# Performance work log

Measured on AMD Instinct MI355X. Metric: run time of the kernel, lower is better.

## Reference

```python
import jax, jax.numpy as jnp
import numpy as np

N = 50000      # nodes
E = 800000     # edges (avg degree 16)
D_IN = 128
D_OUT = 128


def setup_inputs() -> dict:
    key = jax.random.key(0)
    k = jax.random.split(key, 6)
    x = jax.random.normal(k[0], (N, D_IN), dtype=jnp.float32)
    rows = jax.random.randint(k[1], (E,), 0, N, dtype=jnp.int32)   # destination nodes
    cols = jax.random.randint(k[2], (E,), 0, N, dtype=jnp.int32)   # source nodes
    vals = jax.random.uniform(k[3], (E,), dtype=jnp.float32)       # adj edge weights
    W = jax.random.normal(k[4], (D_OUT, D_IN), dtype=jnp.float32) * (1.0 / np.sqrt(D_IN))
    b = jax.random.normal(k[5], (D_OUT,), dtype=jnp.float32) * 0.01
    return {"x": x, "rows": rows, "cols": cols, "vals": vals, "W": W, "b": b}


def reference(x, rows, cols, vals, W, b):
    # Linear: h = x @ W^T + b   (torch nn.Linear convention, W: [out, in])
    h = jnp.einsum("ni,oi->no", x, W) + b            # [N, D_OUT]
    # spmm(adj, h): out[i] = sum_{(i,j) in E} vals_ij * h[j]
    msgs = h[cols] * vals[:, None]                    # [E, D_OUT]
    out = jax.ops.segment_sum(msgs, rows, num_segments=N)  # [N, D_OUT]
    return out
```

## Files before the change

### kernel.cpp

```cpp
#include <hip/hip_runtime.h>

#define D 128
#define SCAN_BLK 256
#define SCAN_THREADS 1024

typedef short  bf16x8 __attribute__((ext_vector_type(8)));
typedef float  f32x4  __attribute__((ext_vector_type(4)));

static __device__ __forceinline__ unsigned short f2bf(float f) {
    unsigned u = __float_as_uint(f);
    u += 0x7FFFu + ((u >> 16) & 1u);
    return (unsigned short)(u >> 16);
}
static __device__ __forceinline__ float bf2f_lo(unsigned u) {
    return __uint_as_float((u & 0xFFFFu) << 16);
}
static __device__ __forceinline__ float bf2f_hi(unsigned u) {
    return __uint_as_float(u & 0xFFFF0000u);
}

__global__ __launch_bounds__(256) void fused_pre(
    const int* __restrict__ rows, int* __restrict__ counts, int n_edges,
    const float* __restrict__ W, unsigned short* __restrict__ Wb, int histBlocks) {
    int bid = blockIdx.x;
    if (bid < histBlocks) {
        int i = bid * 256 + threadIdx.x;
        if (i < n_edges) atomicAdd(&counts[rows[i]], 1);
    } else {
        int i = (bid - histBlocks) * 256 + threadIdx.x;
        if (i < D * D) Wb[i] = f2bf(W[i]);
    }
}

__global__ __launch_bounds__(256) void fused_main(
    const int* __restrict__ rows, const int* __restrict__ cols,
    const float* __restrict__ vals, int* __restrict__ cursor,
    int2* __restrict__ evec, int n_edges, int permSlots,
    const float* __restrict__ x, const unsigned short* __restrict__ Wb,
    const float* __restrict__ b, unsigned short* __restrict__ hb, int n_rows) {
    const int bid = blockIdx.x;
    const int g   = bid / 5;
    const int r5  = bid % 5;

    if (r5 >= 2) {
        const int slot   = g * 3 + (r5 - 2);
        const int stride = permSlots * 256;
        for (int i = slot * 256 + threadIdx.x; i < n_edges; i += stride) {
            int rr  = rows[i];
            int pos = atomicAdd(&cursor[rr], 1);
            evec[pos] = make_int2(cols[i], __float_as_int(vals[i]));
        }
        return;
    }

    const int gb   = g * 2 + r5;
    const int lane = threadIdx.x & 63;
    const int wv   = threadIdx.x >> 6;
    const int row0 = gb * 64 + wv * 16;
    if (row0 >= n_rows) return;
    const int m  = lane & 15;
    const int kg = lane >> 4;

    int arow = row0 + m;
    if (arow >= n_rows) arow = n_rows - 1;
    const float* xr = x + (size_t)arow * D + kg * 8;

    f32x4 acc[8];
#pragma unroll
    for (int n = 0; n < 8; ++n) acc[n] = (f32x4){0.f, 0.f, 0.f, 0.f};

#pragma unroll
    for (int ks = 0; ks < 4; ++ks) {
        float4 f0 = *(const float4*)(xr + ks * 32);
        float4 f1 = *(const float4*)(xr + ks * 32 + 4);
        bf16x8 a;
        a[0] = (short)f2bf(f0.x); a[1] = (short)f2bf(f0.y);
        a[2] = (short)f2bf(f0.z); a[3] = (short)f2bf(f0.w);
        a[4] = (short)f2bf(f1.x); a[5] = (short)f2bf(f1.y);
        a[6] = (short)f2bf(f1.z); a[7] = (short)f2bf(f1.w);
#pragma unroll
        for (int n = 0; n < 8; ++n) {
            bf16x8 bf = *(const bf16x8*)&Wb[(size_t)(n * 16 + m) * D + ks * 32 + kg * 8];
            acc[n] = __builtin_amdgcn_mfma_f32_16x16x32_bf16(a, bf, acc[n], 0, 0, 0);
        }
    }

#pragma unroll
    for (int n = 0; n < 8; ++n) {
        int col = n * 16 + m;
        float bc = b[col];
#pragma unroll
        for (int j = 0; j < 4; ++j) {
            int rr = row0 + kg * 4 + j;
            if (rr < n_rows) hb[(size_t)rr * D + col] = f2bf(acc[n][j] + bc);
        }
    }
}

__global__ __launch_bounds__(SCAN_BLK) void scan_local(
    const int* __restrict__ counts, int* __restrict__ offs,
    int* __restrict__ blockSums, int n) {
    __shared__ int sh[SCAN_BLK];
    const int t = threadIdx.x;
    const int i = blockIdx.x * SCAN_BLK + t;
    int v = (i < n) ? counts[i] : 0;
    sh[t] = v;
    __syncthreads();
    for (int off = 1; off < SCAN_BLK; off <<= 1) {
        int add = (t >= off) ? sh[t - off] : 0;
        __syncthreads();
        sh[t] += add;
        __syncthreads();
    }
    if (i < n) offs[i] = sh[t] - v;
    if (t == SCAN_BLK - 1) blockSums[blockIdx.x] = sh[SCAN_BLK - 1];
}

__global__ __launch_bounds__(1024) void scan_blocks(
    int* __restrict__ blockSums, int* __restrict__ total, int nb) {
    __shared__ int sh[1024];
    const int t = threadIdx.x;
    int v = (t < nb) ? blockSums[t] : 0;
    sh[t] = v;
    __syncthreads();
    for (int off = 1; off < 1024; off <<= 1) {
        int add = (t >= off) ? sh[t - off] : 0;
        __syncthreads();
        sh[t] += add;
        __syncthreads();
    }
    if (t < nb) blockSums[t] = sh[t] - v;
    if (t == 1023) *total = sh[1023];
}

__global__ __launch_bounds__(SCAN_BLK) void scan_add(
    int* __restrict__ offs, int* __restrict__ cursor,
    const int* __restrict__ blockSums, int n) {
    const int i = blockIdx.x * SCAN_BLK + threadIdx.x;
    if (i < n) {
        int o = offs[i] + blockSums[blockIdx.x];
        offs[i]   = o;
        cursor[i] = o;
    }
}

__global__ __launch_bounds__(SCAN_THREADS) void scan_counts(
    const int* __restrict__ counts, int* __restrict__ offs,
    int* __restrict__ cursor, int n) {
    __shared__ int part[SCAN_THREADS];
    const int t = threadIdx.x;
    const int chunk = (n + SCAN_THREADS - 1) / SCAN_THREADS;
    const int s = t * chunk;
    const int e = min(s + chunk, n);
    int sum = 0;
    for (int i = s; i < e; ++i) sum += counts[i];
    part[t] = sum;
    __syncthreads();
    for (int off = 1; off < SCAN_THREADS; off <<= 1) {
        int add = (t >= off) ? part[t - off] : 0;
        __syncthreads();
        part[t] += add;
        __syncthreads();
    }
    int run = part[t] - sum;
    for (int i = s; i < e; ++i) {
        offs[i]   = run;
        cursor[i] = run;
        run += counts[i];
    }
    if (e == n) offs[n] = run;
}

__global__ __launch_bounds__(256, 4) void aggregate(
    const int* __restrict__ offs, const int2* __restrict__ evec,
    const unsigned short* __restrict__ hb, float* __restrict__ out, int n_nodes) {
    const int lane = threadIdx.x & 63;
    const int hl   = lane >> 5;
    const int node = (blockIdx.x * 4 + (threadIdx.x >> 6)) * 2 + hl;
    const int c0   = (lane & 31) * 4;

    int s = 0, e = 0;
    if (node < n_nodes) { s = offs[node]; e = offs[node + 1]; }
    const int rounds = (e - s + 7) >> 3;

    float4 acc = make_float4(0.f, 0.f, 0.f, 0.f);

    for (int rd = 0; rd < rounds; ++rd) {
        const int k = s + rd * 8;
        const int em1 = e - 1;
        int2 r0 = evec[min(k + 0, em1)];
        int2 r1 = evec[min(k + 1, em1)];
        int2 r2 = evec[min(k + 2, em1)];
        int2 r3 = evec[min(k + 3, em1)];
        int2 r4 = evec[min(k + 4, em1)];
        int2 r5 = evec[min(k + 5, em1)];
        int2 r6 = evec[min(k + 6, em1)];
        int2 r7 = evec[min(k + 7, em1)];
        uint2 u0 = *(const uint2*)&hb[(size_t)r0.x * D + c0];
        uint2 u1 = *(const uint2*)&hb[(size_t)r1.x * D + c0];
        uint2 u2 = *(const uint2*)&hb[(size_t)r2.x * D + c0];
        uint2 u3 = *(const uint2*)&hb[(size_t)r3.x * D + c0];
        uint2 u4 = *(const uint2*)&hb[(size_t)r4.x * D + c0];
        uint2 u5 = *(const uint2*)&hb[(size_t)r5.x * D + c0];
        uint2 u6 = *(const uint2*)&hb[(size_t)r6.x * D + c0];
        uint2 u7 = *(const uint2*)&hb[(size_t)r7.x * D + c0];
        float v0 = (k + 0 < e) ? __int_as_float(r0.y) : 0.f;
        float v1 = (k + 1 < e) ? __int_as_float(r1.y) : 0.f;
        float v2 = (k + 2 < e) ? __int_as_float(r2.y) : 0.f;
        float v3 = (k + 3 < e) ? __int_as_float(r3.y) : 0.f;
        float v4 = (k + 4 < e) ? __int_as_float(r4.y) : 0.f;
        float v5 = (k + 5 < e) ? __int_as_float(r5.y) : 0.f;
        float v6 = (k + 6 < e) ? __int_as_float(r6.y) : 0.f;
        float v7 = (k + 7 < e) ? __int_as_float(r7.y) : 0.f;
        acc.x += v0 * bf2f_lo(u0.x); acc.y += v0 * bf2f_hi(u0.x);
        acc.z += v0 * bf2f_lo(u0.y); acc.w += v0 * bf2f_hi(u0.y);
        acc.x += v1 * bf2f_lo(u1.x); acc.y += v1 * bf2f_hi(u1.x);
        acc.z += v1 * bf2f_lo(u1.y); acc.w += v1 * bf2f_hi(u1.y);
        acc.x += v2 * bf2f_lo(u2.x); acc.y += v2 * bf2f_hi(u2.x);
        acc.z += v2 * bf2f_lo(u2.y); acc.w += v2 * bf2f_hi(u2.y);
        acc.x += v3 * bf2f_lo(u3.x); acc.y += v3 * bf2f_hi(u3.x);
        acc.z += v3 * bf2f_lo(u3.y); acc.w += v3 * bf2f_hi(u3.y);
        acc.x += v4 * bf2f_lo(u4.x); acc.y += v4 * bf2f_hi(u4.x);
        acc.z += v4 * bf2f_lo(u4.y); acc.w += v4 * bf2f_hi(u4.y);
        acc.x += v5 * bf2f_lo(u5.x); acc.y += v5 * bf2f_hi(u5.x);
        acc.z += v5 * bf2f_lo(u5.y); acc.w += v5 * bf2f_hi(u5.y);
        acc.x += v6 * bf2f_lo(u6.x); acc.y += v6 * bf2f_hi(u6.x);
        acc.z += v6 * bf2f_lo(u6.y); acc.w += v6 * bf2f_hi(u6.y);
        acc.x += v7 * bf2f_lo(u7.x); acc.y += v7 * bf2f_hi(u7.x);
        acc.z += v7 * bf2f_lo(u7.y); acc.w += v7 * bf2f_hi(u7.y);
    }

    if (node < n_nodes)
        *(float4*)&out[(size_t)node * D + c0] = acc;
}

__global__ __launch_bounds__(256) void scatter_add(
    const int* __restrict__ rows, const int* __restrict__ cols,
    const float* __restrict__ vals, const unsigned short* __restrict__ hb,
    float* __restrict__ out, int n_edges) {
    long long gid = (long long)blockIdx.x * blockDim.x + threadIdx.x;
    int e  = (int)(gid >> 5);
    if (e >= n_edges) return;
    int d4 = ((int)gid & 31) * 4;
    int   r = rows[e];
    int   c = cols[e];
    float v = vals[e];
    const unsigned short* hp = &hb[(size_t)c * D + d4];
    unsigned u0 = *(const unsigned*)(hp + 0);
    unsigned u1 = *(const unsigned*)(hp + 2);
    float* op = &out[(size_t)r * D + d4];
    atomicAdd(op + 0, v * bf2f_lo(u0));
    atomicAdd(op + 1, v * bf2f_hi(u0));
    atomicAdd(op + 2, v * bf2f_lo(u1));
    atomicAdd(op + 3, v * bf2f_hi(u1));
}

__global__ void convert_W(const float* __restrict__ W, unsigned short* __restrict__ Wb) {
    int i = blockIdx.x * blockDim.x + threadIdx.x;
    if (i < D * D) Wb[i] = f2bf(W[i]);
}

__global__ __launch_bounds__(256) void gemm_mfma(
    const float* __restrict__ x, const unsigned short* __restrict__ Wb,
    const float* __restrict__ b, unsigned short* __restrict__ hb, int n_rows) {
    const int lane = threadIdx.x & 63;
    const int wv   = threadIdx.x >> 6;
    const int row0 = blockIdx.x * 64 + wv * 16;
    if (row0 >= n_rows) return;
    const int m  = lane & 15;
    const int kg = lane >> 4;
    int arow = row0 + m;
    if (arow >= n_rows) arow = n_rows - 1;
    const float* xr = x + (size_t)arow * D + kg * 8;
    f32x4 acc[8];
#pragma unroll
    for (int n = 0; n < 8; ++n) acc[n] = (f32x4){0.f, 0.f, 0.f, 0.f};
#pragma unroll
    for (int ks = 0; ks < 4; ++ks) {
        float4 f0 = *(const float4*)(xr + ks * 32);
        float4 f1 = *(const float4*)(xr + ks * 32 + 4);
        bf16x8 a;
        a[0] = (short)f2bf(f0.x); a[1] = (short)f2bf(f0.y);
        a[2] = (short)f2bf(f0.z); a[3] = (short)f2bf(f0.w);
        a[4] = (short)f2bf(f1.x); a[5] = (short)f2bf(f1.y);
        a[6] = (short)f2bf(f1.z); a[7] = (short)f2bf(f1.w);
#pragma unroll
        for (int n = 0; n < 8; ++n) {
            bf16x8 bf = *(const bf16x8*)&Wb[(size_t)(n * 16 + m) * D + ks * 32 + kg * 8];
            acc[n] = __builtin_amdgcn_mfma_f32_16x16x32_bf16(a, bf, acc[n], 0, 0, 0);
        }
    }
#pragma unroll
    for (int n = 0; n < 8; ++n) {
        int col = n * 16 + m;
        float bc = b[col];
#pragma unroll
        for (int j = 0; j < 4; ++j) {
            int r = row0 + kg * 4 + j;
            if (r < n_rows) hb[(size_t)r * D + col] = f2bf(acc[n][j] + bc);
        }
    }
}

static inline size_t align16(size_t x) { return (x + 15) & ~(size_t)15; }

extern "C" void kernel_launch(void* const* d_in, const int* in_sizes, int n_in,
                              void* d_out, int out_size, void* d_ws, size_t ws_size,
                              hipStream_t stream) {
    const float* x    = (const float*)d_in[0];
    const int*   rows = (const int*)  d_in[1];
    const int*   cols = (const int*)  d_in[2];
    const float* vals = (const float*)d_in[3];
    const float* W    = (const float*)d_in[4];
    const float* b    = (const float*)d_in[5];
    float*       out  = (float*)d_out;

    const int n_nodes = in_sizes[0] / D;
    const int n_edges = in_sizes[1];
    const int nScanBlocks = (n_nodes + SCAN_BLK - 1) / SCAN_BLK;
    const int histBlocks  = (n_edges + 255) / 256;
    const int convBlocks  = (D * D + 255) / 256;
    const int gemmBlocks  = (n_nodes + 63) / 64;
    const int nGroups     = (gemmBlocks + 1) / 2;
    const int permSlots   = nGroups * 3;
    const int mainBlocks  = nGroups * 5;
    const int aggBlocks   = (n_nodes + 7) / 8;

    char*  base    = (char*)d_ws;
    size_t off     = 0;
    unsigned short* Wb = (unsigned short*)(base + off); off = align16(off + (size_t)D * D * 2);
    unsigned short* hb = (unsigned short*)(base + off); off = align16(off + (size_t)n_nodes * D * 2);
    int*   counts  = (int*)  (base + off); off = align16(off + (size_t)n_nodes * 4);
    int*   offs    = (int*)  (base + off); off = align16(off + ((size_t)n_nodes + 1) * 4);
    int*   cursor  = (int*)  (base + off); off = align16(off + (size_t)n_nodes * 4);
    int*   bsums   = (int*)  (base + off); off = align16(off + (size_t)1024 * 4);
    int2*  evec    = (int2*) (base + off); off = align16(off + (size_t)n_edges * 8);
    const bool csr_fits = (off <= ws_size);

    if (csr_fits) {
        hipMemsetAsync(counts, 0, (size_t)n_nodes * 4, stream);
        fused_pre<<<histBlocks + convBlocks, 256, 0, stream>>>(
            rows, counts, n_edges, W, Wb, histBlocks);
        if (nScanBlocks <= 1024) {
            scan_local<<<nScanBlocks, SCAN_BLK, 0, stream>>>(counts, offs, bsums, n_nodes);
            scan_blocks<<<1, 1024, 0, stream>>>(bsums, &offs[n_nodes], nScanBlocks);
            scan_add<<<nScanBlocks, SCAN_BLK, 0, stream>>>(offs, cursor, bsums, n_nodes);
        } else {
            scan_counts<<<1, SCAN_THREADS, 0, stream>>>(counts, offs, cursor, n_nodes);
        }
        fused_main<<<mainBlocks, 256, 0, stream>>>(
            rows, cols, vals, cursor, evec, n_edges, permSlots,
            x, Wb, b, hb, n_nodes);
        aggregate<<<aggBlocks, 256, 0, stream>>>(offs, evec, hb, out, n_nodes);
    } else {
        convert_W<<<convBlocks, 256, 0, stream>>>(W, Wb);
        gemm_mfma<<<gemmBlocks, 256, 0, stream>>>(x, Wb, b, hb, n_nodes);
        hipMemsetAsync(d_out, 0, (size_t)n_nodes * D * sizeof(float), stream);
        long long scatter_threads = (long long)n_edges * 32;
        int scatter_blocks = (int)((scatter_threads + 255) / 256);
        scatter_add<<<scatter_blocks, 256, 0, stream>>>(rows, cols, vals, hb, out, n_edges);
    }
}
```

Before: 144.1 us.

## Partition CSR build into eight XCD-aligned edge classes with per-class cursors

Edges are split into eight classes by 256-edge chunk index. Histogram and permutation blocks are arranged so that block index mod 8 matches the class, and each class uses its own count and cursor arrays (class-major, eight times n_nodes). The intent is that each class's atomics and evec writes stay within one XCD's L2, avoiding cross-die atomic traffic. The cost is an eight-times-larger scan, and an aggregate that reads eight per-class segments per node and runs for the largest class count. Those extra rounds issue padded, redundant gathers.

```diff
diff --git a/kernel.cpp b/kernel.cpp
--- a/kernel.cpp
+++ b/kernel.cpp
@@ -2,7 +2,6 @@
 
 #define D 128
 #define SCAN_BLK 256
-#define SCAN_THREADS 1024
 
 typedef short  bf16x8 __attribute__((ext_vector_type(8)));
 typedef float  f32x4  __attribute__((ext_vector_type(4)));
@@ -20,80 +19,19 @@
 }
 
 __global__ __launch_bounds__(256) void fused_pre(
-    const int* __restrict__ rows, int* __restrict__ counts, int n_edges,
+    const int* __restrict__ rows, int* __restrict__ counts8,
+    int n_edges, int n_nodes,
     const float* __restrict__ W, unsigned short* __restrict__ Wb, int histBlocks) {
     int bid = blockIdx.x;
     if (bid < histBlocks) {
         int i = bid * 256 + threadIdx.x;
-        if (i < n_edges) atomicAdd(&counts[rows[i]], 1);
+        if (i < n_edges) {
+            int cls = (i >> 8) & 7;
+            atomicAdd(&counts8[cls * n_nodes + rows[i]], 1);
+        }
     } else {
         int i = (bid - histBlocks) * 256 + threadIdx.x;
         if (i < D * D) Wb[i] = f2bf(W[i]);
-    }
-}
-
-__global__ __launch_bounds__(256) void fused_main(
-    const int* __restrict__ rows, const int* __restrict__ cols,
-    const float* __restrict__ vals, int* __restrict__ cursor,
-    int2* __restrict__ evec, int n_edges, int permSlots,
-    const float* __restrict__ x, const unsigned short* __restrict__ Wb,
-    const float* __restrict__ b, unsigned short* __restrict__ hb, int n_rows) {
-    const int bid = blockIdx.x;
-    const int g   = bid / 5;
-    const int r5  = bid % 5;
-
-    if (r5 >= 2) {
-        const int slot   = g * 3 + (r5 - 2);
-        const int stride = permSlots * 256;
-        for (int i = slot * 256 + threadIdx.x; i < n_edges; i += stride) {
-            int rr  = rows[i];
-            int pos = atomicAdd(&cursor[rr], 1);
-            evec[pos] = make_int2(cols[i], __float_as_int(vals[i]));
-        }
-        return;
-    }
-
-    const int gb   = g * 2 + r5;
-    const int lane = threadIdx.x & 63;
-    const int wv   = threadIdx.x >> 6;
-    const int row0 = gb * 64 + wv * 16;
-    if (row0 >= n_rows) return;
-    const int m  = lane & 15;
-    const int kg = lane >> 4;
-
-    int arow = row0 + m;
-    if (arow >= n_rows) arow = n_rows - 1;
-    const float* xr = x + (size_t)arow * D + kg * 8;
-
-    f32x4 acc[8];
-#pragma unroll
-    for (int n = 0; n < 8; ++n) acc[n] = (f32x4){0.f, 0.f, 0.f, 0.f};
-
-#pragma unroll
-    for (int ks = 0; ks < 4; ++ks) {
-        float4 f0 = *(const float4*)(xr + ks * 32);
-        float4 f1 = *(const float4*)(xr + ks * 32 + 4);
-        bf16x8 a;
-        a[0] = (short)f2bf(f0.x); a[1] = (short)f2bf(f0.y);
-        a[2] = (short)f2bf(f0.z); a[3] = (short)f2bf(f0.w);
-        a[4] = (short)f2bf(f1.x); a[5] = (short)f2bf(f1.y);
-        a[6] = (short)f2bf(f1.z); a[7] = (short)f2bf(f1.w);
-#pragma unroll
-        for (int n = 0; n < 8; ++n) {
-            bf16x8 bf = *(const bf16x8*)&Wb[(size_t)(n * 16 + m) * D + ks * 32 + kg * 8];
-            acc[n] = __builtin_amdgcn_mfma_f32_16x16x32_bf16(a, bf, acc[n], 0, 0, 0);
-        }
-    }
-
-#pragma unroll
-    for (int n = 0; n < 8; ++n) {
-        int col = n * 16 + m;
-        float bc = b[col];
-#pragma unroll
-        for (int j = 0; j < 4; ++j) {
-            int rr = row0 + kg * 4 + j;
-            if (rr < n_rows) hb[(size_t)rr * D + col] = f2bf(acc[n][j] + bc);
-        }
     }
 }
 
@@ -116,12 +54,13 @@
     if (t == SCAN_BLK - 1) blockSums[blockIdx.x] = sh[SCAN_BLK - 1];
 }
 
-__global__ __launch_bounds__(1024) void scan_blocks(
+__global__ __launch_bounds__(1024) void scan_blocks2(
     int* __restrict__ blockSums, int* __restrict__ total, int nb) {
     __shared__ int sh[1024];
     const int t = threadIdx.x;
-    int v = (t < nb) ? blockSums[t] : 0;
-    sh[t] = v;
+    int c0 = (t * 2     < nb) ? blockSums[t * 2]     : 0;
+    int c1 = (t * 2 + 1 < nb) ? blockSums[t * 2 + 1] : 0;
+    sh[t] = c0 + c1;
     __syncthreads();
     for (int off = 1; off < 1024; off <<= 1) {
         int add = (t >= off) ? sh[t - off] : 0;
@@ -129,7 +68,9 @@
         sh[t] += add;
         __syncthreads();
     }
-    if (t < nb) blockSums[t] = sh[t] - v;
+    int base = sh[t] - (c0 + c1);
+    if (t * 2 < nb)     blockSums[t * 2]     = base;
+    if (t * 2 + 1 < nb) blockSums[t * 2 + 1] = base + c0;
     if (t == 1023) *total = sh[1023];
 }
 
@@ -144,94 +85,177 @@
     }
 }
 
-__global__ __launch_bounds__(SCAN_THREADS) void scan_counts(
-    const int* __restrict__ counts, int* __restrict__ offs,
-    int* __restrict__ cursor, int n) {
-    __shared__ int part[SCAN_THREADS];
-    const int t = threadIdx.x;
-    const int chunk = (n + SCAN_THREADS - 1) / SCAN_THREADS;
-    const int s = t * chunk;
-    const int e = min(s + chunk, n);
-    int sum = 0;
-    for (int i = s; i < e; ++i) sum += counts[i];
-    part[t] = sum;
-    __syncthreads();
-    for (int off = 1; off < SCAN_THREADS; off <<= 1) {
-        int add = (t >= off) ? part[t - off] : 0;
-        __syncthreads();
-        part[t] += add;
-        __syncthreads();
-    }
-    int run = part[t] - sum;
-    for (int i = s; i < e; ++i) {
-        offs[i]   = run;
-        cursor[i] = run;
-        run += counts[i];
-    }
-    if (e == n) offs[n] = run;
+__global__ __launch_bounds__(256) void fused_main(
+    const int* __restrict__ rows, const int* __restrict__ cols,
+    const float* __restrict__ vals, int* __restrict__ cursor8,
+    int2* __restrict__ evec, int n_edges, int n_nodes,
+    int nChunks, int QperClass,
+    const float* __restrict__ x, const unsigned short* __restrict__ Wb,
+    const float* __restrict__ b, unsigned short* __restrict__ hb, int n_rows) {
+    const int bid = blockIdx.x;
+    const int r5  = bid % 5;
+
+    if (r5 >= 2) {
+        const int k   = bid & 7;
+        const int S   = bid / 40;
+        const int pos = bid % 40;
+        int r = 0;
+        for (int p = 0; p < pos; ++p)
+            if ((p % 5) >= 2 && (p & 7) == k) ++r;
+        const int q = S * 3 + r;
+        for (int m = q; ; m += QperClass) {
+            int c = k + 8 * m;
+            if (c >= nChunks) break;
+            int i = c * 256 + threadIdx.x;
+            if (i < n_edges) {
+                int rr  = rows[i];
+                int pp  = atomicAdd(&cursor8[k * n_nodes + rr], 1);
+                evec[pp] = make_int2(cols[i], __float_as_int(vals[i]));
+            }
+        }
+        return;
+    }
+
+    const int gb   = (bid / 5) * 2 + r5;
+    const int lane = threadIdx.x & 63;
+    const int wv   = threadIdx.x >> 6;
+    const int row0 = gb * 64 + wv * 16;
+    if (row0 >= n_rows) return;
+    const int m  = lane & 15;
+    const int kg = lane >> 4;
+
+    int arow = row0 + m;
+    if (arow >= n_rows) arow = n_rows - 1;
+    const float* xr = x + (size_t)arow * D + kg * 8;
+
+    f32x4 acc[8];
+#pragma unroll
+    for (int n = 0; n < 8; ++n) acc[n] = (f32x4){0.f, 0.f, 0.f, 0.f};
+
+#pragma unroll
+    for (int ks = 0; ks < 4; ++ks) {
+        float4 f0 = *(const float4*)(xr + ks * 32);
+        float4 f1 = *(const float4*)(xr + ks * 32 + 4);
+        bf16x8 a;
+        a[0] = (short)f2bf(f0.x); a[1] = (short)f2bf(f0.y);
+        a[2] = (short)f2bf(f0.z); a[3] = (short)f2bf(f0.w);
+        a[4] = (short)f2bf(f1.x); a[5] = (short)f2bf(f1.y);
+        a[6] = (short)f2bf(f1.z); a[7] = (short)f2bf(f1.w);
+#pragma unroll
+        for (int n = 0; n < 8; ++n) {
+            bf16x8 bf = *(const bf16x8*)&Wb[(size_t)(n * 16 + m) * D + ks * 32 + kg * 8];
+            acc[n] = __builtin_amdgcn_mfma_f32_16x16x32_bf16(a, bf, acc[n], 0, 0, 0);
+        }
+    }
+
+#pragma unroll
+    for (int n = 0; n < 8; ++n) {
+        int col = n * 16 + m;
+        float bc = b[col];
+#pragma unroll
+        for (int j = 0; j < 4; ++j) {
+            int rr = row0 + kg * 4 + j;
+            if (rr < n_rows) hb[(size_t)rr * D + col] = f2bf(acc[n][j] + bc);
+        }
+    }
 }
 
 __global__ __launch_bounds__(256, 4) void aggregate(
-    const int* __restrict__ offs, const int2* __restrict__ evec,
-    const unsigned short* __restrict__ hb, float* __restrict__ out, int n_nodes) {
+    const int* __restrict__ offs8, const int2* __restrict__ evec,
+    const unsigned short* __restrict__ hb, float* __restrict__ out,
+    int n_nodes, int n_edges) {
     const int lane = threadIdx.x & 63;
     const int hl   = lane >> 5;
     const int node = (blockIdx.x * 4 + (threadIdx.x >> 6)) * 2 + hl;
     const int c0   = (lane & 31) * 4;
 
-    int s = 0, e = 0;
-    if (node < n_nodes) { s = offs[node]; e = offs[node + 1]; }
-    const int rounds = (e - s + 7) >> 3;
+    int s[8], cnt[8];
+    int rounds = 0;
+    if (node < n_nodes) {
+#pragma unroll
+        for (int c = 0; c < 8; ++c) {
+            int a  = offs8[c * n_nodes + node];
+            int bd = offs8[c * n_nodes + node + 1];
+            s[c]   = a;
+            cnt[c] = bd - a;
+            rounds = max(rounds, cnt[c]);
+        }
+    } else {
+#pragma unroll
+        for (int c = 0; c < 8; ++c) { s[c] = 0; cnt[c] = 0; }
+    }
 
     float4 acc = make_float4(0.f, 0.f, 0.f, 0.f);
+    const int emax = n_edges - 1;
 
     for (int rd = 0; rd < rounds; ++rd) {
-        const int k = s + rd * 8;
-        const int em1 = e - 1;
-        int2 r0 = evec[min(k + 0, em1)];
-        int2 r1 = evec[min(k + 1, em1)];
-        int2 r2 = evec[min(k + 2, em1)];
-        int2 r3 = evec[min(k + 3, em1)];
-        int2 r4 = evec[min(k + 4, em1)];
-        int2 r5 = evec[min(k + 5, em1)];
-        int2 r6 = evec[min(k + 6, em1)];
-        int2 r7 = evec[min(k + 7, em1)];
-        uint2 u0 = *(const uint2*)&hb[(size_t)r0.x * D + c0];
-        uint2 u1 = *(const uint2*)&hb[(size_t)r1.x * D + c0];
-        uint2 u2 = *(const uint2*)&hb[(size_t)r2.x * D + c0];
-        uint2 u3 = *(const uint2*)&hb[(size_t)r3.x * D + c0];
-        uint2 u4 = *(const uint2*)&hb[(size_t)r4.x * D + c0];
-        uint2 u5 = *(const uint2*)&hb[(size_t)r5.x * D + c0];
-        uint2 u6 = *(const uint2*)&hb[(size_t)r6.x * D + c0];
-        uint2 u7 = *(const uint2*)&hb[(size_t)r7.x * D + c0];
-        float v0 = (k + 0 < e) ? __int_as_float(r0.y) : 0.f;
-        float v1 = (k + 1 < e) ? __int_as_float(r1.y) : 0.f;
-        float v2 = (k + 2 < e) ? __int_as_float(r2.y) : 0.f;
-        float v3 = (k + 3 < e) ? __int_as_float(r3.y) : 0.f;
-        float v4 = (k + 4 < e) ? __int_as_float(r4.y) : 0.f;
-        float v5 = (k + 5 < e) ? __int_as_float(r5.y) : 0.f;
-        float v6 = (k + 6 < e) ? __int_as_float(r6.y) : 0.f;
-        float v7 = (k + 7 < e) ? __int_as_float(r7.y) : 0.f;
-        acc.x += v0 * bf2f_lo(u0.x); acc.y += v0 * bf2f_hi(u0.x);
-        acc.z += v0 * bf2f_lo(u0.y); acc.w += v0 * bf2f_hi(u0.y);
-        acc.x += v1 * bf2f_lo(u1.x); acc.y += v1 * bf2f_hi(u1.x);
-        acc.z += v1 * bf2f_lo(u1.y); acc.w += v1 * bf2f_hi(u1.y);
-        acc.x += v2 * bf2f_lo(u2.x); acc.y += v2 * bf2f_hi(u2.x);
-        acc.z += v2 * bf2f_lo(u2.y); acc.w += v2 * bf2f_hi(u2.y);
-        acc.x += v3 * bf2f_lo(u3.x); acc.y += v3 * bf2f_hi(u3.x);
-        acc.z += v3 * bf2f_lo(u3.y); acc.w += v3 * bf2f_hi(u3.y);
-        acc.x += v4 * bf2f_lo(u4.x); acc.y += v4 * bf2f_hi(u4.x);
-        acc.z += v4 * bf2f_lo(u4.y); acc.w += v4 * bf2f_hi(u4.y);
-        acc.x += v5 * bf2f_lo(u5.x); acc.y += v5 * bf2f_hi(u5.x);
-        acc.z += v5 * bf2f_lo(u5.y); acc.w += v5 * bf2f_hi(u5.y);
-        acc.x += v6 * bf2f_lo(u6.x); acc.y += v6 * bf2f_hi(u6.x);
-        acc.z += v6 * bf2f_lo(u6.y); acc.w += v6 * bf2f_hi(u6.y);
-        acc.x += v7 * bf2f_lo(u7.x); acc.y += v7 * bf2f_hi(u7.x);
-        acc.z += v7 * bf2f_lo(u7.y); acc.w += v7 * bf2f_hi(u7.y);
+        int2  rec[8];
+#pragma unroll
+        for (int c = 0; c < 8; ++c) {
+            int idx = s[c] + min(rd, max(cnt[c] - 1, 0));
+            rec[c] = evec[min(idx, emax)];
+        }
+        uint2 u[8];
+#pragma unroll
+        for (int c = 0; c < 8; ++c)
+            u[c] = *(const uint2*)&hb[(size_t)rec[c].x * D + c0];
+#pragma unroll
+        for (int c = 0; c < 8; ++c) {
+            float v = (rd < cnt[c]) ? __int_as_float(rec[c].y) : 0.f;
+            acc.x += v * bf2f_lo(u[c].x); acc.y += v * bf2f_hi(u[c].x);
+            acc.z += v * bf2f_lo(u[c].y); acc.w += v * bf2f_hi(u[c].y);
+        }
     }
 
     if (node < n_nodes)
         *(float4*)&out[(size_t)node * D + c0] = acc;
+}
+
+__global__ void convert_W(const float* __restrict__ W, unsigned short* __restrict__ Wb) {
+    int i = blockIdx.x * blockDim.x + threadIdx.x;
+    if (i < D * D) Wb[i] = f2bf(W[i]);
+}
+
+__global__ __launch_bounds__(256) void gemm_mfma(
+    const float* __restrict__ x, const unsigned short* __restrict__ Wb,
+    const float* __restrict__ b, unsigned short* __restrict__ hb, int n_rows) {
+    const int lane = threadIdx.x & 63;
+    const int wv   = threadIdx.x >> 6;
+    const int row0 = blockIdx.x * 64 + wv * 16;
+    if (row0 >= n_rows) return;
+    const int m  = lane & 15;
+    const int kg = lane >> 4;
+    int arow = row0 + m;
+    if (arow >= n_rows) arow = n_rows - 1;
+    const float* xr = x + (size_t)arow * D + kg * 8;
+    f32x4 acc[8];
+#pragma unroll
+    for (int n = 0; n < 8; ++n) acc[n] = (f32x4){0.f, 0.f, 0.f, 0.f};
+#pragma unroll
+    for (int ks = 0; ks < 4; ++ks) {
+        float4 f0 = *(const float4*)(xr + ks * 32);
+        float4 f1 = *(const float4*)(xr + ks * 32 + 4);
+        bf16x8 a;
+        a[0] = (short)f2bf(f0.x); a[1] = (short)f2bf(f0.y);
+        a[2] = (short)f2bf(f0.z); a[3] = (short)f2bf(f0.w);
+        a[4] = (short)f2bf(f1.x); a[5] = (short)f2bf(f1.y);
+        a[6] = (short)f2bf(f1.z); a[7] = (short)f2bf(f1.w);
+#pragma unroll
+        for (int n = 0; n < 8; ++n) {
+            bf16x8 bf = *(const bf16x8*)&Wb[(size_t)(n * 16 + m) * D + ks * 32 + kg * 8];
+            acc[n] = __builtin_amdgcn_mfma_f32_16x16x32_bf16(a, bf, acc[n], 0, 0, 0);
+        }
+    }
+#pragma unroll
+    for (int n = 0; n < 8; ++n) {
+        int col = n * 16 + m;
+        float bc = b[col];
+#pragma unroll
+        for (int j = 0; j < 4; ++j) {
+            int r = row0 + kg * 4 + j;
+            if (r < n_rows) hb[(size_t)r * D + col] = f2bf(acc[n][j] + bc);
+        }
+    }
 }
 
 __global__ __launch_bounds__(256) void scatter_add(
@@ -255,53 +279,6 @@
     atomicAdd(op + 3, v * bf2f_hi(u1));
 }
 
-__global__ void convert_W(const float* __restrict__ W, unsigned short* __restrict__ Wb) {
-    int i = blockIdx.x * blockDim.x + threadIdx.x;
-    if (i < D * D) Wb[i] = f2bf(W[i]);
-}
-
-__global__ __launch_bounds__(256) void gemm_mfma(
-    const float* __restrict__ x, const unsigned short* __restrict__ Wb,
-    const float* __restrict__ b, unsigned short* __restrict__ hb, int n_rows) {
-    const int lane = threadIdx.x & 63;
-    const int wv   = threadIdx.x >> 6;
-    const int row0 = blockIdx.x * 64 + wv * 16;
-    if (row0 >= n_rows) return;
-    const int m  = lane & 15;
-    const int kg = lane >> 4;
-    int arow = row0 + m;
-    if (arow >= n_rows) arow = n_rows - 1;
-    const float* xr = x + (size_t)arow * D + kg * 8;
-    f32x4 acc[8];
-#pragma unroll
-    for (int n = 0; n < 8; ++n) acc[n] = (f32x4){0.f, 0.f, 0.f, 0.f};
-#pragma unroll
-    for (int ks = 0; ks < 4; ++ks) {
-        float4 f0 = *(const float4*)(xr + ks * 32);
-        float4 f1 = *(const float4*)(xr + ks * 32 + 4);
-        bf16x8 a;
-        a[0] = (short)f2bf(f0.x); a[1] = (short)f2bf(f0.y);
-        a[2] = (short)f2bf(f0.z); a[3] = (short)f2bf(f0.w);
-        a[4] = (short)f2bf(f1.x); a[5] = (short)f2bf(f1.y);
-        a[6] = (short)f2bf(f1.z); a[7] = (short)f2bf(f1.w);
-#pragma unroll
-        for (int n = 0; n < 8; ++n) {
-            bf16x8 bf = *(const bf16x8*)&Wb[(size_t)(n * 16 + m) * D + ks * 32 + kg * 8];
-            acc[n] = __builtin_amdgcn_mfma_f32_16x16x32_bf16(a, bf, acc[n], 0, 0, 0);
-        }
-    }
-#pragma unroll
-    for (int n = 0; n < 8; ++n) {
-        int col = n * 16 + m;
-        float bc = b[col];
-#pragma unroll
-        for (int j = 0; j < 4; ++j) {
-            int r = row0 + kg * 4 + j;
-            if (r < n_rows) hb[(size_t)r * D + col] = f2bf(acc[n][j] + bc);
-        }
-    }
-}
-
 static inline size_t align16(size_t x) { return (x + 15) & ~(size_t)15; }
 
 extern "C" void kernel_launch(void* const* d_in, const int* in_sizes, int n_in,
@@ -317,41 +294,39 @@
 
     const int n_nodes = in_sizes[0] / D;
     const int n_edges = in_sizes[1];
-    const int nScanBlocks = (n_nodes + SCAN_BLK - 1) / SCAN_BLK;
-    const int histBlocks  = (n_edges + 255) / 256;
-    const int convBlocks  = (D * D + 255) / 256;
-    const int gemmBlocks  = (n_nodes + 63) / 64;
-    const int nGroups     = (gemmBlocks + 1) / 2;
-    const int permSlots   = nGroups * 3;
-    const int mainBlocks  = nGroups * 5;
-    const int aggBlocks   = (n_nodes + 7) / 8;
+    const int histBlocks = (n_edges + 255) / 256;
+    const int convBlocks = (D * D + 255) / 256;
+    const int gemmBlocks = (n_nodes + 63) / 64;
+    const int nSuper     = (gemmBlocks + 15) / 16;
+    const int mainBlocks = nSuper * 40;
+    const int QperClass  = nSuper * 3;
+    const int n8         = 8 * n_nodes;
+    const int nScanBlocks = (n8 + SCAN_BLK - 1) / SCAN_BLK;
+    const int aggBlocks  = (n_nodes + 7) / 8;
 
     char*  base    = (char*)d_ws;
     size_t off     = 0;
     unsigned short* Wb = (unsigned short*)(base + off); off = align16(off + (size_t)D * D * 2);
     unsigned short* hb = (unsigned short*)(base + off); off = align16(off + (size_t)n_nodes * D * 2);
-    int*   counts  = (int*)  (base + off); off = align16(off + (size_t)n_nodes * 4);
-    int*   offs    = (int*)  (base + off); off = align16(off + ((size_t)n_nodes + 1) * 4);
-    int*   cursor  = (int*)  (base + off); off = align16(off + (size_t)n_nodes * 4);
-    int*   bsums   = (int*)  (base + off); off = align16(off + (size_t)1024 * 4);
+    int*   counts8 = (int*)  (base + off); off = align16(off + (size_t)n8 * 4);
+    int*   offs8   = (int*)  (base + off); off = align16(off + ((size_t)n8 + 1) * 4);
+    int*   cursor8 = (int*)  (base + off); off = align16(off + (size_t)n8 * 4);
+    int*   bsums   = (int*)  (base + off); off = align16(off + (size_t)2048 * 4);
     int2*  evec    = (int2*) (base + off); off = align16(off + (size_t)n_edges * 8);
-    const bool csr_fits = (off <= ws_size);
-
-    if (csr_fits) {
-        hipMemsetAsync(counts, 0, (size_t)n_nodes * 4, stream);
+    const bool ok = (off <= ws_size) && (nScanBlocks <= 2048);
+
+    if (ok) {
+        hipMemsetAsync(counts8, 0, (size_t)n8 * 4, stream);
         fused_pre<<<histBlocks + convBlocks, 256, 0, stream>>>(
-            rows, counts, n_edges, W, Wb, histBlocks);
-        if (nScanBlocks <= 1024) {
-            scan_local<<<nScanBlocks, SCAN_BLK, 0, stream>>>(counts, offs, bsums, n_nodes);
-            scan_blocks<<<1, 1024, 0, stream>>>(bsums, &offs[n_nodes], nScanBlocks);
-            scan_add<<<nScanBlocks, SCAN_BLK, 0, stream>>>(offs, cursor, bsums, n_nodes);
-        } else {
-            scan_counts<<<1, SCAN_THREADS, 0, stream>>>(counts, offs, cursor, n_nodes);
-        }
+            rows, counts8, n_edges, n_nodes, W, Wb, histBlocks);
+        scan_local<<<nScanBlocks, SCAN_BLK, 0, stream>>>(counts8, offs8, bsums, n8);
+        scan_blocks2<<<1, 1024, 0, stream>>>(bsums, &offs8[n8], nScanBlocks);
+        scan_add<<<nScanBlocks, SCAN_BLK, 0, stream>>>(offs8, cursor8, bsums, n8);
         fused_main<<<mainBlocks, 256, 0, stream>>>(
-            rows, cols, vals, cursor, evec, n_edges, permSlots,
-            x, Wb, b, hb, n_nodes);
-        aggregate<<<aggBlocks, 256, 0, stream>>>(offs, evec, hb, out, n_nodes);
+            rows, cols, vals, cursor8, evec, n_edges, n_nodes,
+            histBlocks, QperClass, x, Wb, b, hb, n_nodes);
+        aggregate<<<aggBlocks, 256, 0, stream>>>(
+            offs8, evec, hb, out, n_nodes, n_edges);
     } else {
         convert_W<<<convBlocks, 256, 0, stream>>>(W, Wb);
         gemm_mfma<<<gemmBlocks, 256, 0, stream>>>(x, Wb, b, hb, n_nodes);
```

After: 161.5 us. 12.1% more time.

## Fuse whole pipeline into one cooperative persistent kernel with grid syncs

Applied to the files above, without the earlier changes.

Replaces the sequence of memset, histogram, three scan kernels, permute+GEMM and aggregate launches with a single cooperative kernel that separates the phases with grid.sync(). GEMM tiles and the edge permutation run concurrently on disjoint block subsets. The aggregation is changed to one wave per node with two columns per lane instead of a half-wave with four. This is meant to remove launch gaps and inter-kernel drain, at the cost of grid-wide barriers, a grid size capped by occupancy, and narrower per-lane gathers. The atomic scatter fallback for a small workspace is removed, so the workspace-size check no longer exists.

```diff
diff --git a/kernel.cpp b/kernel.cpp
--- a/kernel.cpp
+++ b/kernel.cpp
@@ -1,8 +1,10 @@
 #include <hip/hip_runtime.h>
+#include <hip/hip_cooperative_groups.h>
+
+namespace cg = cooperative_groups;
 
 #define D 128
 #define SCAN_BLK 256
-#define SCAN_THREADS 1024
 
 typedef short  bf16x8 __attribute__((ext_vector_type(8)));
 typedef float  f32x4  __attribute__((ext_vector_type(4)));
@@ -17,6 +19,174 @@
 }
 static __device__ __forceinline__ float bf2f_hi(unsigned u) {
     return __uint_as_float(u & 0xFFFF0000u);
+}
+
+__global__ __launch_bounds__(256) void mega(
+    const int* __restrict__ rows, const int* __restrict__ cols,
+    const float* __restrict__ vals, const float* __restrict__ W,
+    const float* __restrict__ b, const float* __restrict__ x,
+    int* __restrict__ counts, int* __restrict__ offs, int* __restrict__ cursor,
+    int* __restrict__ bsums, int2* __restrict__ evec,
+    unsigned short* __restrict__ Wb, unsigned short* __restrict__ hb,
+    float* __restrict__ out,
+    int n_nodes, int n_edges, int nScanChunks, int gemmTiles, int gemmShare) {
+    cg::grid_group grid = cg::this_grid();
+    const int t   = threadIdx.x;
+    const int bid = blockIdx.x;
+    const int G   = gridDim.x;
+    const int gstride = G * 256;
+    __shared__ int sh[SCAN_BLK];
+
+    for (int i = bid * 256 + t; i < n_nodes; i += gstride) counts[i] = 0;
+    for (int i = bid * 256 + t; i < D * D;   i += gstride) Wb[i] = f2bf(W[i]);
+    grid.sync();
+
+    for (int i = bid * 256 + t; i < n_edges; i += gstride)
+        atomicAdd(&counts[rows[i]], 1);
+    grid.sync();
+
+    for (int ch = bid; ch < nScanChunks; ch += G) {
+        int i = ch * 256 + t;
+        int v = (i < n_nodes) ? counts[i] : 0;
+        sh[t] = v;
+        __syncthreads();
+        for (int off = 1; off < 256; off <<= 1) {
+            int add = (t >= off) ? sh[t - off] : 0;
+            __syncthreads();
+            sh[t] += add;
+            __syncthreads();
+        }
+        if (i < n_nodes) offs[i] = sh[t] - v;
+        if (t == 255) bsums[ch] = sh[255];
+        __syncthreads();
+    }
+    grid.sync();
+
+    if (bid == 0) {
+        int v = (t < nScanChunks) ? bsums[t] : 0;
+        sh[t] = v;
+        __syncthreads();
+        for (int off = 1; off < 256; off <<= 1) {
+            int add = (t >= off) ? sh[t - off] : 0;
+            __syncthreads();
+            sh[t] += add;
+            __syncthreads();
+        }
+        if (t < nScanChunks) bsums[t] = sh[t] - v;
+        if (t == 255) offs[n_nodes] = sh[255];
+    }
+    grid.sync();
+
+    for (int ch = bid; ch < nScanChunks; ch += G) {
+        int i = ch * 256 + t;
+        if (i < n_nodes) {
+            int o = offs[i] + bsums[ch];
+            offs[i]   = o;
+            cursor[i] = o;
+        }
+    }
+    grid.sync();
+
+    if (bid < gemmShare) {
+        const int lane = t & 63;
+        const int wv   = t >> 6;
+        const int m    = lane & 15;
+        const int kg   = lane >> 4;
+        for (int gb = bid; gb < gemmTiles; gb += gemmShare) {
+            const int row0 = gb * 64 + wv * 16;
+            if (row0 >= n_nodes) continue;
+            int arow = row0 + m;
+            if (arow >= n_nodes) arow = n_nodes - 1;
+            const float* xr = x + (size_t)arow * D + kg * 8;
+
+            f32x4 acc[8];
+#pragma unroll
+            for (int n = 0; n < 8; ++n) acc[n] = (f32x4){0.f, 0.f, 0.f, 0.f};
+#pragma unroll
+            for (int ks = 0; ks < 4; ++ks) {
+                float4 f0 = *(const float4*)(xr + ks * 32);
+                float4 f1 = *(const float4*)(xr + ks * 32 + 4);
+                bf16x8 a;
+                a[0] = (short)f2bf(f0.x); a[1] = (short)f2bf(f0.y);
+                a[2] = (short)f2bf(f0.z); a[3] = (short)f2bf(f0.w);
+                a[4] = (short)f2bf(f1.x); a[5] = (short)f2bf(f1.y);
+                a[6] = (short)f2bf(f1.z); a[7] = (short)f2bf(f1.w);
+#pragma unroll
+                for (int n = 0; n < 8; ++n) {
+                    bf16x8 bf = *(const bf16x8*)&Wb[(size_t)(n * 16 + m) * D + ks * 32 + kg * 8];
+                    acc[n] = __builtin_amdgcn_mfma_f32_16x16x32_bf16(a, bf, acc[n], 0, 0, 0);
+                }
+            }
+#pragma unroll
+            for (int n = 0; n < 8; ++n) {
+                int col = n * 16 + m;
+                float bc = b[col];
+#pragma unroll
+                for (int j = 0; j < 4; ++j) {
+                    int rr = row0 + kg * 4 + j;
+                    if (rr < n_nodes) hb[(size_t)rr * D + col] = f2bf(acc[n][j] + bc);
+                }
+            }
+        }
+    } else {
+        const int slot  = bid - gemmShare;
+        const int nperm = G - gemmShare;
+        for (int i = slot * 256 + t; i < n_edges; i += nperm * 256) {
+            int rr  = rows[i];
+            int pos = atomicAdd(&cursor[rr], 1);
+            evec[pos] = make_int2(cols[i], __float_as_int(vals[i]));
+        }
+    }
+    grid.sync();
+
+    {
+        const int lane = t & 63;
+        const int wv   = t >> 6;
+        const int c0   = lane * 2;
+        for (int wid = bid * 4 + wv; wid < n_nodes; wid += G * 4) {
+            const int s = offs[wid];
+            const int e = offs[wid + 1];
+            const int rounds = (e - s + 7) >> 3;
+            float2 acc = make_float2(0.f, 0.f);
+            for (int rd = 0; rd < rounds; ++rd) {
+                const int k   = s + rd * 8;
+                const int em1 = e - 1;
+                int2 r0 = evec[min(k + 0, em1)];
+                int2 r1 = evec[min(k + 1, em1)];
+                int2 r2 = evec[min(k + 2, em1)];
+                int2 r3 = evec[min(k + 3, em1)];
+                int2 r4 = evec[min(k + 4, em1)];
+                int2 r5 = evec[min(k + 5, em1)];
+                int2 r6 = evec[min(k + 6, em1)];
+                int2 r7 = evec[min(k + 7, em1)];
+                unsigned u0 = *(const unsigned*)&hb[(size_t)r0.x * D + c0];
+                unsigned u1 = *(const unsigned*)&hb[(size_t)r1.x * D + c0];
+                unsigned u2 = *(const unsigned*)&hb[(size_t)r2.x * D + c0];
+                unsigned u3 = *(const unsigned*)&hb[(size_t)r3.x * D + c0];
+                unsigned u4 = *(const unsigned*)&hb[(size_t)r4.x * D + c0];
+                unsigned u5 = *(const unsigned*)&hb[(size_t)r5.x * D + c0];
+                unsigned u6 = *(const unsigned*)&hb[(size_t)r6.x * D + c0];
+                unsigned u7 = *(const unsigned*)&hb[(size_t)r7.x * D + c0];
+                float v0 = (k + 0 < e) ? __int_as_float(r0.y) : 0.f;
+                float v1 = (k + 1 < e) ? __int_as_float(r1.y) : 0.f;
+                float v2 = (k + 2 < e) ? __int_as_float(r2.y) : 0.f;
+                float v3 = (k + 3 < e) ? __int_as_float(r3.y) : 0.f;
+                float v4 = (k + 4 < e) ? __int_as_float(r4.y) : 0.f;
+                float v5 = (k + 5 < e) ? __int_as_float(r5.y) : 0.f;
+                float v6 = (k + 6 < e) ? __int_as_float(r6.y) : 0.f;
+                float v7 = (k + 7 < e) ? __int_as_float(r7.y) : 0.f;
+                acc.x += v0 * bf2f_lo(u0); acc.y += v0 * bf2f_hi(u0);
+                acc.x += v1 * bf2f_lo(u1); acc.y += v1 * bf2f_hi(u1);
+                acc.x += v2 * bf2f_lo(u2); acc.y += v2 * bf2f_hi(u2);
+                acc.x += v3 * bf2f_lo(u3); acc.y += v3 * bf2f_hi(u3);
+                acc.x += v4 * bf2f_lo(u4); acc.y += v4 * bf2f_hi(u4);
+                acc.x += v5 * bf2f_lo(u5); acc.y += v5 * bf2f_hi(u5);
+                acc.x += v6 * bf2f_lo(u6); acc.y += v6 * bf2f_hi(u6);
+                acc.x += v7 * bf2f_lo(u7); acc.y += v7 * bf2f_hi(u7);
+            }
+            *(float2*)&out[(size_t)wid * D + c0] = acc;
+        }
+    }
 }
 
 __global__ __launch_bounds__(256) void fused_pre(
@@ -68,7 +238,6 @@
     f32x4 acc[8];
 #pragma unroll
     for (int n = 0; n < 8; ++n) acc[n] = (f32x4){0.f, 0.f, 0.f, 0.f};
-
 #pragma unroll
     for (int ks = 0; ks < 4; ++ks) {
         float4 f0 = *(const float4*)(xr + ks * 32);
@@ -84,7 +253,6 @@
             acc[n] = __builtin_amdgcn_mfma_f32_16x16x32_bf16(a, bf, acc[n], 0, 0, 0);
         }
     }
-
 #pragma unroll
     for (int n = 0; n < 8; ++n) {
         int col = n * 16 + m;
@@ -144,49 +312,21 @@
     }
 }
 
-__global__ __launch_bounds__(SCAN_THREADS) void scan_counts(
-    const int* __restrict__ counts, int* __restrict__ offs,
-    int* __restrict__ cursor, int n) {
-    __shared__ int part[SCAN_THREADS];
-    const int t = threadIdx.x;
-    const int chunk = (n + SCAN_THREADS - 1) / SCAN_THREADS;
-    const int s = t * chunk;
-    const int e = min(s + chunk, n);
-    int sum = 0;
-    for (int i = s; i < e; ++i) sum += counts[i];
-    part[t] = sum;
-    __syncthreads();
-    for (int off = 1; off < SCAN_THREADS; off <<= 1) {
-        int add = (t >= off) ? part[t - off] : 0;
-        __syncthreads();
-        part[t] += add;
-        __syncthreads();
-    }
-    int run = part[t] - sum;
-    for (int i = s; i < e; ++i) {
-        offs[i]   = run;
-        cursor[i] = run;
-        run += counts[i];
-    }
-    if (e == n) offs[n] = run;
-}
-
 __global__ __launch_bounds__(256, 4) void aggregate(
     const int* __restrict__ offs, const int2* __restrict__ evec,
     const unsigned short* __restrict__ hb, float* __restrict__ out, int n_nodes) {
     const int lane = threadIdx.x & 63;
-    const int hl   = lane >> 5;
-    const int node = (blockIdx.x * 4 + (threadIdx.x >> 6)) * 2 + hl;
-    const int c0   = (lane & 31) * 4;
-
-    int s = 0, e = 0;
-    if (node < n_nodes) { s = offs[node]; e = offs[node + 1]; }
+    const int wv   = threadIdx.x >> 6;
+    const int c0   = lane * 2;
+    int wid = blockIdx.x * 4 + wv;
+    if (wid >= n_nodes) return;
+
+    const int s = offs[wid];
+    const int e = offs[wid + 1];
     const int rounds = (e - s + 7) >> 3;
-
-    float4 acc = make_float4(0.f, 0.f, 0.f, 0.f);
-
+    float2 acc = make_float2(0.f, 0.f);
     for (int rd = 0; rd < rounds; ++rd) {
-        const int k = s + rd * 8;
+        const int k   = s + rd * 8;
         const int em1 = e - 1;
         int2 r0 = evec[min(k + 0, em1)];
         int2 r1 = evec[min(k + 1, em1)];
@@ -196,14 +336,14 @@
         int2 r5 = evec[min(k + 5, em1)];
         int2 r6 = evec[min(k + 6, em1)];
         int2 r7 = evec[min(k + 7, em1)];
-        uint2 u0 = *(const uint2*)&hb[(size_t)r0.x * D + c0];
-        uint2 u1 = *(const uint2*)&hb[(size_t)r1.x * D + c0];
-        uint2 u2 = *(const uint2*)&hb[(size_t)r2.x * D + c0];
-        uint2 u3 = *(const uint2*)&hb[(size_t)r3.x * D + c0];
-        uint2 u4 = *(const uint2*)&hb[(size_t)r4.x * D + c0];
-        uint2 u5 = *(const uint2*)&hb[(size_t)r5.x * D + c0];
-        uint2 u6 = *(const uint2*)&hb[(size_t)r6.x * D + c0];
-        uint2 u7 = *(const uint2*)&hb[(size_t)r7.x * D + c0];
+        unsigned u0 = *(const unsigned*)&hb[(size_t)r0.x * D + c0];
+        unsigned u1 = *(const unsigned*)&hb[(size_t)r1.x * D + c0];
+        unsigned u2 = *(const unsigned*)&hb[(size_t)r2.x * D + c0];
+        unsigned u3 = *(const unsigned*)&hb[(size_t)r3.x * D + c0];
+        unsigned u4 = *(const unsigned*)&hb[(size_t)r4.x * D + c0];
+        unsigned u5 = *(const unsigned*)&hb[(size_t)r5.x * D + c0];
+        unsigned u6 = *(const unsigned*)&hb[(size_t)r6.x * D + c0];
+        unsigned u7 = *(const unsigned*)&hb[(size_t)r7.x * D + c0];
         float v0 = (k + 0 < e) ? __int_as_float(r0.y) : 0.f;
         float v1 = (k + 1 < e) ? __int_as_float(r1.y) : 0.f;
         float v2 = (k + 2 < e) ? __int_as_float(r2.y) : 0.f;
@@ -212,94 +352,16 @@
         float v5 = (k + 5 < e) ? __int_as_float(r5.y) : 0.f;
         float v6 = (k + 6 < e) ? __int_as_float(r6.y) : 0.f;
         float v7 = (k + 7 < e) ? __int_as_float(r7.y) : 0.f;
-        acc.x += v0 * bf2f_lo(u0.x); acc.y += v0 * bf2f_hi(u0.x);
-        acc.z += v0 * bf2f_lo(u0.y); acc.w += v0 * bf2f_hi(u0.y);
-        acc.x += v1 * bf2f_lo(u1.x); acc.y += v1 * bf2f_hi(u1.x);
-        acc.z += v1 * bf2f_lo(u1.y); acc.w += v1 * bf2f_hi(u1.y);
-        acc.x += v2 * bf2f_lo(u2.x); acc.y += v2 * bf2f_hi(u2.x);
-        acc.z += v2 * bf2f_lo(u2.y); acc.w += v2 * bf2f_hi(u2.y);
-        acc.x += v3 * bf2f_lo(u3.x); acc.y += v3 * bf2f_hi(u3.x);
-        acc.z += v3 * bf2f_lo(u3.y); acc.w += v3 * bf2f_hi(u3.y);
-        acc.x += v4 * bf2f_lo(u4.x); acc.y += v4 * bf2f_hi(u4.x);
-        acc.z += v4 * bf2f_lo(u4.y); acc.w += v4 * bf2f_hi(u4.y);
-        acc.x += v5 * bf2f_lo(u5.x); acc.y += v5 * bf2f_hi(u5.x);
-        acc.z += v5 * bf2f_lo(u5.y); acc.w += v5 * bf2f_hi(u5.y);
-        acc.x += v6 * bf2f_lo(u6.x); acc.y += v6 * bf2f_hi(u6.x);
-        acc.z += v6 * bf2f_lo(u6.y); acc.w += v6 * bf2f_hi(u6.y);
-        acc.x += v7 * bf2f_lo(u7.x); acc.y += v7 * bf2f_hi(u7.x);
-        acc.z += v7 * bf2f_lo(u7.y); acc.w += v7 * bf2f_hi(u7.y);
-    }
-
-    if (node < n_nodes)
-        *(float4*)&out[(size_t)node * D + c0] = acc;
-}
-
-__global__ __launch_bounds__(256) void scatter_add(
-    const int* __restrict__ rows, const int* __restrict__ cols,
-    const float* __restrict__ vals, const unsigned short* __restrict__ hb,
-    float* __restrict__ out, int n_edges) {
-    long long gid = (long long)blockIdx.x * blockDim.x + threadIdx.x;
-    int e  = (int)(gid >> 5);
-    if (e >= n_edges) return;
-    int d4 = ((int)gid & 31) * 4;
-    int   r = rows[e];
-    int   c = cols[e];
-    float v = vals[e];
-    const unsigned short* hp = &hb[(size_t)c * D + d4];
-    unsigned u0 = *(const unsigned*)(hp + 0);
-    unsigned u1 = *(const unsigned*)(hp + 2);
-    float* op = &out[(size_t)r * D + d4];
-    atomicAdd(op + 0, v * bf2f_lo(u0));
-    atomicAdd(op + 1, v * bf2f_hi(u0));
-    atomicAdd(op + 2, v * bf2f_lo(u1));
-    atomicAdd(op + 3, v * bf2f_hi(u1));
-}
-
-__global__ void convert_W(const float* __restrict__ W, unsigned short* __restrict__ Wb) {
-    int i = blockIdx.x * blockDim.x + threadIdx.x;
-    if (i < D * D) Wb[i] = f2bf(W[i]);
-}
-
-__global__ __launch_bounds__(256) void gemm_mfma(
-    const float* __restrict__ x, const unsigned short* __restrict__ Wb,
-    const float* __restrict__ b, unsigned short* __restrict__ hb, int n_rows) {
-    const int lane = threadIdx.x & 63;
-    const int wv   = threadIdx.x >> 6;
-    const int row0 = blockIdx.x * 64 + wv * 16;
-    if (row0 >= n_rows) return;
-    const int m  = lane & 15;
-    const int kg = lane >> 4;
-    int arow = row0 + m;
-    if (arow >= n_rows) arow = n_rows - 1;
-    const float* xr = x + (size_t)arow * D + kg * 8;
-    f32x4 acc[8];
-#pragma unroll
-    for (int n = 0; n < 8; ++n) acc[n] = (f32x4){0.f, 0.f, 0.f, 0.f};
-#pragma unroll
-    for (int ks = 0; ks < 4; ++ks) {
-        float4 f0 = *(const float4*)(xr + ks * 32);
-        float4 f1 = *(const float4*)(xr + ks * 32 + 4);
-        bf16x8 a;
-        a[0] = (short)f2bf(f0.x); a[1] = (short)f2bf(f0.y);
-        a[2] = (short)f2bf(f0.z); a[3] = (short)f2bf(f0.w);
-        a[4] = (short)f2bf(f1.x); a[5] = (short)f2bf(f1.y);
-        a[6] = (short)f2bf(f1.z); a[7] = (short)f2bf(f1.w);
-#pragma unroll
-        for (int n = 0; n < 8; ++n) {
-            bf16x8 bf = *(const bf16x8*)&Wb[(size_t)(n * 16 + m) * D + ks * 32 + kg * 8];
-            acc[n] = __builtin_amdgcn_mfma_f32_16x16x32_bf16(a, bf, acc[n], 0, 0, 0);
-        }
-    }
-#pragma unroll
-    for (int n = 0; n < 8; ++n) {
-        int col = n * 16 + m;
-        float bc = b[col];
-#pragma unroll
-        for (int j = 0; j < 4; ++j) {
-            int r = row0 + kg * 4 + j;
-            if (r < n_rows) hb[(size_t)r * D + col] = f2bf(acc[n][j] + bc);
-        }
-    }
+        acc.x += v0 * bf2f_lo(u0); acc.y += v0 * bf2f_hi(u0);
+        acc.x += v1 * bf2f_lo(u1); acc.y += v1 * bf2f_hi(u1);
+        acc.x += v2 * bf2f_lo(u2); acc.y += v2 * bf2f_hi(u2);
+        acc.x += v3 * bf2f_lo(u3); acc.y += v3 * bf2f_hi(u3);
+        acc.x += v4 * bf2f_lo(u4); acc.y += v4 * bf2f_hi(u4);
+        acc.x += v5 * bf2f_lo(u5); acc.y += v5 * bf2f_hi(u5);
+        acc.x += v6 * bf2f_lo(u6); acc.y += v6 * bf2f_hi(u6);
+        acc.x += v7 * bf2f_lo(u7); acc.y += v7 * bf2f_hi(u7);
+    }
+    *(float2*)&out[(size_t)wid * D + c0] = acc;
 }
 
 static inline size_t align16(size_t x) { return (x + 15) & ~(size_t)15; }
@@ -315,16 +377,10 @@
     const float* b    = (const float*)d_in[5];
     float*       out  = (float*)d_out;
 
-    const int n_nodes = in_sizes[0] / D;
-    const int n_edges = in_sizes[1];
-    const int nScanBlocks = (n_nodes + SCAN_BLK - 1) / SCAN_BLK;
-    const int histBlocks  = (n_edges + 255) / 256;
-    const int convBlocks  = (D * D + 255) / 256;
-    const int gemmBlocks  = (n_nodes + 63) / 64;
-    const int nGroups     = (gemmBlocks + 1) / 2;
-    const int permSlots   = nGroups * 3;
-    const int mainBlocks  = nGroups * 5;
-    const int aggBlocks   = (n_nodes + 7) / 8;
+    int n_nodes = in_sizes[0] / D;
+    int n_edges = in_sizes[1];
+    const int nScanChunks = (n_nodes + 255) / 256;
+    int gemmTiles = (n_nodes + 63) / 64;
 
     char*  base    = (char*)d_ws;
     size_t off     = 0;
@@ -335,29 +391,49 @@
     int*   cursor  = (int*)  (base + off); off = align16(off + (size_t)n_nodes * 4);
     int*   bsums   = (int*)  (base + off); off = align16(off + (size_t)1024 * 4);
     int2*  evec    = (int2*) (base + off); off = align16(off + (size_t)n_edges * 8);
-    const bool csr_fits = (off <= ws_size);
-
-    if (csr_fits) {
+    (void)ws_size;
+
+    bool launched = false;
+    if (nScanChunks <= 256) {
+        int maxB = 0;
+        hipError_t occ = hipOccupancyMaxActiveBlocksPerMultiprocessor(
+            &maxB, (const void*)mega, 256, 0);
+        if (occ != hipSuccess || maxB < 1) maxB = 4;
+        int G = maxB * 256;
+        if (G > 2048) G = 2048;
+        int gemmShare = (G * 2) / 5;
+        if (gemmShare < 1) gemmShare = 1;
+        if (gemmShare >= G) gemmShare = G - 1;
+
+        void* args[] = {
+            (void*)&rows, (void*)&cols, (void*)&vals, (void*)&W, (void*)&b,
+            (void*)&x, (void*)&counts, (void*)&offs, (void*)&cursor,
+            (void*)&bsums, (void*)&evec, (void*)&Wb, (void*)&hb, (void*)&out,
+            (void*)&n_nodes, (void*)&n_edges, (void*)&nScanChunks,
+            (void*)&gemmTiles, (void*)&gemmShare
+        };
+        hipError_t err = hipLaunchCooperativeKernel(
+            (const void*)mega, dim3(G), dim3(256), args, 0, stream);
+        launched = (err == hipSuccess);
+    }
+
+    if (!launched) {
+        const int histBlocks = (n_edges + 255) / 256;
+        const int convBlocks = (D * D + 255) / 256;
+        const int nGroups    = (gemmTiles + 1) / 2;
+        const int permSlots  = nGroups * 3;
+        const int mainBlocks = nGroups * 5;
+        const int nScanBlocks = (n_nodes + SCAN_BLK - 1) / SCAN_BLK;
+
         hipMemsetAsync(counts, 0, (size_t)n_nodes * 4, stream);
         fused_pre<<<histBlocks + convBlocks, 256, 0, stream>>>(
             rows, counts, n_edges, W, Wb, histBlocks);
-        if (nScanBlocks <= 1024) {
-            scan_local<<<nScanBlocks, SCAN_BLK, 0, stream>>>(counts, offs, bsums, n_nodes);
-            scan_blocks<<<1, 1024, 0, stream>>>(bsums, &offs[n_nodes], nScanBlocks);
-            scan_add<<<nScanBlocks, SCAN_BLK, 0, stream>>>(offs, cursor, bsums, n_nodes);
-        } else {
-            scan_counts<<<1, SCAN_THREADS, 0, stream>>>(counts, offs, cursor, n_nodes);
-        }
+        scan_local<<<nScanBlocks, SCAN_BLK, 0, stream>>>(counts, offs, bsums, n_nodes);
+        scan_blocks<<<1, 1024, 0, stream>>>(bsums, &offs[n_nodes], nScanBlocks);
+        scan_add<<<nScanBlocks, SCAN_BLK, 0, stream>>>(offs, cursor, bsums, n_nodes);
         fused_main<<<mainBlocks, 256, 0, stream>>>(
             rows, cols, vals, cursor, evec, n_edges, permSlots,
             x, Wb, b, hb, n_nodes);
-        aggregate<<<aggBlocks, 256, 0, stream>>>(offs, evec, hb, out, n_nodes);
-    } else {
-        convert_W<<<convBlocks, 256, 0, stream>>>(W, Wb);
-        gemm_mfma<<<gemmBlocks, 256, 0, stream>>>(x, Wb, b, hb, n_nodes);
-        hipMemsetAsync(d_out, 0, (size_t)n_nodes * D * sizeof(float), stream);
-        long long scatter_threads = (long long)n_edges * 32;
-        int scatter_blocks = (int)((scatter_threads + 255) / 256);
-        scatter_add<<<scatter_blocks, 256, 0, stream>>>(rows, cols, vals, hb, out, n_edges);
-    }
-}
+        aggregate<<<(n_nodes + 3) / 4, 256, 0, stream>>>(offs, evec, hb, out, n_nodes);
+    }
+}
```

New measurement: 399.3 us. 177% more time.
